# Kernel tuning notes

Hardware: AMD Instinct MI355X
Metric: run time of the kernel (lower is better)

## Reference

```python
import jax, jax.numpy as jnp
import numpy as np

B, N, D = 4, 1024, 1024
H = 16
HD = D // H
FF = int(D * 2.0)
EPS = 1e-5


def setup_inputs() -> dict:
    key = jax.random.key(0)
    ks = jax.random.split(key, 12)
    s = lambda fan_in: 1.0 / np.sqrt(fan_in)
    return {
        "x": jax.random.normal(ks[0], (B, N, D), dtype=jnp.float32),
        "ln1_g": jnp.ones((D,), jnp.float32),
        "ln1_b": jnp.zeros((D,), jnp.float32),
        "qkv_w": jax.random.normal(ks[1], (D, 3 * D), jnp.float32) * s(D),
        "qkv_b": jnp.zeros((3 * D,), jnp.float32),
        "out_w": jax.random.normal(ks[2], (D, D), jnp.float32) * s(D),
        "out_b": jnp.zeros((D,), jnp.float32),
        "ln2_g": jnp.ones((D,), jnp.float32),
        "ln2_b": jnp.zeros((D,), jnp.float32),
        "w1": jax.random.normal(ks[3], (D, FF), jnp.float32) * s(D),
        "b1": jnp.zeros((FF,), jnp.float32),
        "w2": jax.random.normal(ks[4], (FF, D), jnp.float32) * s(FF),
        "b2": jnp.zeros((D,), jnp.float32),
    }


def _layernorm(x, g, b):
    mu = jnp.mean(x, axis=-1, keepdims=True)
    var = jnp.mean(jnp.square(x - mu), axis=-1, keepdims=True)
    return (x - mu) * jax.lax.rsqrt(var + EPS) * g + b


def _attention(x, qkv_w, qkv_b, out_w, out_b):
    qkv = x @ qkv_w + qkv_b                       # (B,N,3D)
    qkv = qkv.reshape(B, N, 3, H, HD)
    q, k, v = qkv[:, :, 0], qkv[:, :, 1], qkv[:, :, 2]  # (B,N,H,HD)
    scale = 1.0 / np.sqrt(HD)
    attn = jnp.einsum("bnhd,bmhd->bhnm", q, k) * scale
    attn = jax.nn.softmax(attn, axis=-1)
    out = jnp.einsum("bhnm,bmhd->bnhd", attn, v).reshape(B, N, D)
    return out @ out_w + out_b


def reference(x, ln1_g, ln1_b, qkv_w, qkv_b, out_w, out_b, ln2_g, ln2_b, w1, b1, w2, b2):
    x = x + _attention(_layernorm(x, ln1_g, ln1_b), qkv_w, qkv_b, out_w, out_b)
    h = _layernorm(x, ln2_g, ln2_b)
    h = jax.nn.gelu(h @ w1 + b1, approximate=False) @ w2 + b2
    return x + h
```

## Files before the change

### kernel.cpp

```cpp
#include <hip/hip_runtime.h>
#include <hip/hip_bf16.h>
#include <cstdint>
#include <cstddef>

#define Bq 4
#define Nseq 1024
#define Dm 1024
#define Hh 16
#define HDd 64
#define FFd 2048
#define Mrows 4096

typedef __attribute__((ext_vector_type(8))) short bf16x8;
typedef __attribute__((ext_vector_type(4))) float f32x4;
typedef __attribute__((ext_vector_type(16))) float f32x16;

__device__ __forceinline__ void gl_lds16(const void* g, void* l) {
  __builtin_amdgcn_global_load_lds(
      (const __attribute__((address_space(1))) unsigned int*)g,
      (__attribute__((address_space(3))) unsigned int*)l, 16, 0, 0);
}

__device__ __forceinline__ unsigned short f2b(float f) {
  union { __hip_bfloat16 h; unsigned short u; } cv;
  cv.h = __float2bfloat16(f);
  return cv.u;
}

__device__ __forceinline__ unsigned cvt_pk_bf16(float a, float b) {
  unsigned r;
  asm("v_cvt_pk_bf16_f32 %0, %1, %2" : "=v"(r) : "v"(a), "v"(b));
  return r;
}

__device__ __forceinline__ void pl32_swap(unsigned& a, unsigned& b) {
  asm("v_permlane32_swap_b32 %0, %1" : "+v"(a), "+v"(b));
}

__global__ __launch_bounds__(256) void transpose_cast_k(
    const float* __restrict__ src, __hip_bfloat16* __restrict__ dst,
    int K, int Ncols) {
  __shared__ float tile[32][33];
  const int n0 = blockIdx.x * 32, k0 = blockIdx.y * 32;
  const int tx = threadIdx.x & 31, ty = threadIdx.x >> 5;
#pragma unroll
  for (int i = 0; i < 32; i += 8)
    tile[ty + i][tx] = src[(size_t)(k0 + ty + i) * Ncols + n0 + tx];
  __syncthreads();
#pragma unroll
  for (int i = 0; i < 32; i += 8)
    dst[(size_t)(n0 + ty + i) * K + k0 + tx] = __float2bfloat16(tile[tx][ty + i]);
}

__global__ __launch_bounds__(256) void ln_kernel(
    const float* __restrict__ x, const float* __restrict__ gw,
    const float* __restrict__ bw, __hip_bfloat16* __restrict__ out) {
  const int row = blockIdx.x;
  const float4 v = reinterpret_cast<const float4*>(x + (size_t)row * Dm)[threadIdx.x];
  float s1 = v.x + v.y + v.z + v.w;
  float s2 = v.x * v.x + v.y * v.y + v.z * v.z + v.w * v.w;
#pragma unroll
  for (int m = 1; m < 64; m <<= 1) {
    s1 += __shfl_xor(s1, m);
    s2 += __shfl_xor(s2, m);
  }
  __shared__ float a1[4], a2[4];
  const int wv = threadIdx.x >> 6;
  if ((threadIdx.x & 63) == 0) { a1[wv] = s1; a2[wv] = s2; }
  __syncthreads();
  s1 = a1[0] + a1[1] + a1[2] + a1[3];
  s2 = a2[0] + a2[1] + a2[2] + a2[3];
  const float mu = s1 * (1.f / Dm);
  const float rs = rsqrtf(s2 * (1.f / Dm) - mu * mu + 1e-5f);
  const float4 g4 = reinterpret_cast<const float4*>(gw)[threadIdx.x];
  const float4 b4 = reinterpret_cast<const float4*>(bw)[threadIdx.x];
  ushort4 o;
  o.x = f2b((v.x - mu) * rs * g4.x + b4.x);
  o.y = f2b((v.y - mu) * rs * g4.y + b4.y);
  o.z = f2b((v.z - mu) * rs * g4.z + b4.z);
  o.w = f2b((v.w - mu) * rs * g4.w + b4.w);
  reinterpret_cast<ushort4*>(out + (size_t)row * Dm)[threadIdx.x] = o;
}

template <int EPI>
__global__ __launch_bounds__(256, 3) void gemm_bt(
    const __hip_bfloat16* __restrict__ A, const __hip_bfloat16* __restrict__ BT,
    const float* __restrict__ bias, const float* __restrict__ res,
    float* __restrict__ outF, __hip_bfloat16* __restrict__ outB,
    __hip_bfloat16* __restrict__ qb, __hip_bfloat16* __restrict__ kb,
    __hip_bfloat16* __restrict__ vtb, int Ndim, int Kdim) {
  __shared__ alignas(16) __hip_bfloat16 As[128 * 64];
  __shared__ alignas(16) __hip_bfloat16 Bs[128 * 64];
  const int tid = threadIdx.x;
  const int wv = tid >> 6, ln = tid & 63;
  const int wm = wv >> 1, wn = wv & 1;
  const int lq = ln & 31, hl = ln >> 5;
  const int rowBase = blockIdx.y * 128;
  const int colBase = blockIdx.x * 128;

  const int st_row = tid >> 3;
  const int st_c = (tid & 7) ^ (st_row & 7);

  f32x16 acc[2][2];
#pragma unroll
  for (int i = 0; i < 2; ++i)
#pragma unroll
    for (int j = 0; j < 2; ++j) acc[i][j] = {};

  auto stage = [&](int k0) {
#pragma unroll
    for (int r = 0; r < 4; ++r) {
      gl_lds16(A + (size_t)(rowBase + r * 32 + st_row) * Kdim + k0 + st_c * 8,
               (char*)As + r * 4096 + wv * 1024);
      gl_lds16(BT + (size_t)(colBase + r * 32 + st_row) * Kdim + k0 + st_c * 8,
               (char*)Bs + r * 4096 + wv * 1024);
    }
  };

  const int nt = Kdim >> 6;
  for (int kt = 0; kt < nt; ++kt) {
    stage(kt << 6);
    __syncthreads();
    const char* Ap = (const char*)As;
    const char* Bp = (const char*)Bs;
#pragma unroll
    for (int ks = 0; ks < 4; ++ks) {
      bf16x8 af[2], bfr[2];
#pragma unroll
      for (int i = 0; i < 2; ++i)
        af[i] = *reinterpret_cast<const bf16x8*>(
            Ap + (wm * 64 + i * 32 + lq) * 128 + (((ks * 2 + hl) ^ (lq & 7)) * 16));
#pragma unroll
      for (int j = 0; j < 2; ++j)
        bfr[j] = *reinterpret_cast<const bf16x8*>(
            Bp + (wn * 64 + j * 32 + lq) * 128 + (((ks * 2 + hl) ^ (lq & 7)) * 16));
#pragma unroll
      for (int i = 0; i < 2; ++i)
#pragma unroll
        for (int j = 0; j < 2; ++j)
          acc[i][j] = __builtin_amdgcn_mfma_f32_32x32x16_bf16(af[i], bfr[j], acc[i][j], 0, 0, 0);
    }
    __syncthreads();
  }

#pragma unroll
  for (int i = 0; i < 2; ++i) {
#pragma unroll
    for (int j = 0; j < 2; ++j) {
      const int gc = colBase + wn * 64 + j * 32 + lq;
      const float bv = bias[gc];
#pragma unroll
      for (int r = 0; r < 16; ++r) {
        const int gr = rowBase + wm * 64 + i * 32 + (r & 3) + 8 * (r >> 2) + 4 * hl;
        float v = acc[i][j][r] + bv;
        if constexpr (EPI == 0) {
          const int which = gc >> 10;
          const int dcol = gc & 1023;
          const int h = dcol >> 6, hd = dcol & 63;
          const int b = gr >> 10, n = gr & 1023;
          const size_t bh = (size_t)(b * Hh + h);
          if (which == 0)
            qb[(bh * Nseq + n) * HDd + hd] = __float2bfloat16(v * 0.125f);
          else if (which == 1)
            kb[(bh * Nseq + n) * HDd + hd] = __float2bfloat16(v);
          else
            vtb[(bh * HDd + hd) * Nseq + n] = __float2bfloat16(v);
        } else if constexpr (EPI == 1) {
          outF[(size_t)gr * Ndim + gc] = v + res[(size_t)gr * Ndim + gc];
        } else {
          outB[(size_t)gr * Ndim + gc] =
              __float2bfloat16(0.5f * v * (1.f + erff(v * 0.70710678118f)));
        }
      }
    }
  }
}

__global__ __launch_bounds__(256, 2) void attn_kernel(
    const __hip_bfloat16* __restrict__ q, const __hip_bfloat16* __restrict__ k,
    const __hip_bfloat16* __restrict__ vt, __hip_bfloat16* __restrict__ attn) {
  __shared__ alignas(16) __hip_bfloat16 Ks[2][64 * 64];
  __shared__ alignas(16) __hip_bfloat16 Vs[2][64 * 64];
  const int tid = threadIdx.x, wv = tid >> 6, ln = tid & 63;
  const int bh = blockIdx.x >> 3, qt = blockIdx.x & 7;
  const int b = bh >> 4, h = bh & 15;
  const int lq = ln & 31;
  const int hl = ln >> 5;

  const __hip_bfloat16* kbase = k + (size_t)bh * Nseq * HDd;
  const __hip_bfloat16* vbase = vt + (size_t)bh * HDd * Nseq;

  const int st_r = ln >> 3;
  const int st_c = (ln & 7) ^ st_r;

  const __hip_bfloat16* qsrc = q + ((size_t)bh * Nseq + qt * 128 + wv * 32 + lq) * HDd;
  bf16x8 qf[4];
#pragma unroll
  for (int s = 0; s < 4; ++s)
    qf[s] = *reinterpret_cast<const bf16x8*>(qsrc + s * 16 + hl * 8);

  float mrun = -1e30f, lrun = 0.f;
  f32x16 ot0 = {}, ot1 = {};

  auto stage = [&](int buf, int kt) {
#pragma unroll
    for (int c = 0; c < 2; ++c) {
      const int chunk = wv * 2 + c;
      gl_lds16(kbase + ((size_t)kt * 64 + chunk * 8 + st_r) * HDd + st_c * 8,
               (char*)&Ks[buf][0] + chunk * 1024);
      gl_lds16(vbase + (size_t)(chunk * 8 + st_r) * Nseq + kt * 64 + st_c * 8,
               (char*)&Vs[buf][0] + chunk * 1024);
    }
  };

  stage(0, 0);
  __syncthreads();
  int cur = 0;

  for (int kt = 0; kt < 16; ++kt) {
    if (kt < 15) stage(cur ^ 1, kt + 1);

    const char* Kp = (const char*)&Ks[cur][0];
    const char* Vp = (const char*)&Vs[cur][0];

    f32x16 st0 = {}, st1 = {};
#pragma unroll
    for (int t = 0; t < 2; ++t) {
      const int row = t * 32 + lq;
#pragma unroll
      for (int s = 0; s < 4; ++s) {
        const bf16x8 kf = *reinterpret_cast<const bf16x8*>(
            Kp + row * 128 + (((s * 2 + hl) ^ (row & 7)) * 16));
        if (t == 0) st0 = __builtin_amdgcn_mfma_f32_32x32x16_bf16(kf, qf[s], st0, 0, 0, 0);
        else        st1 = __builtin_amdgcn_mfma_f32_32x32x16_bf16(kf, qf[s], st1, 0, 0, 0);
      }
    }

    float tmax = st0[0];
#pragma unroll
    for (int r = 1; r < 16; ++r) tmax = fmaxf(tmax, st0[r]);
#pragma unroll
    for (int r = 0; r < 16; ++r) tmax = fmaxf(tmax, st1[r]);
    tmax = fmaxf(tmax, __shfl_xor(tmax, 32));
    const float mn = fmaxf(mrun, tmax);
    const float sc = __expf(mrun - mn);
    mrun = mn;
    float tsum = 0.f;
#pragma unroll
    for (int r = 0; r < 16; ++r) {
      st0[r] = __expf(st0[r] - mn);
      tsum += st0[r];
    }
#pragma unroll
    for (int r = 0; r < 16; ++r) {
      st1[r] = __expf(st1[r] - mn);
      tsum += st1[r];
    }
    tsum += __shfl_xor(tsum, 32);
    lrun = lrun * sc + tsum;
#pragma unroll
    for (int r = 0; r < 16; ++r) { ot0[r] *= sc; ot1[r] *= sc; }

    union PF { unsigned u[4]; bf16x8 v; } pf[4];
#pragma unroll
    for (int t = 0; t < 2; ++t)
#pragma unroll
      for (int g = 0; g < 2; ++g) {
        unsigned w0, w1, w2, w3;
        if (t == 0) {
          w0 = cvt_pk_bf16(st0[g * 8 + 0], st0[g * 8 + 1]);
          w1 = cvt_pk_bf16(st0[g * 8 + 2], st0[g * 8 + 3]);
          w2 = cvt_pk_bf16(st0[g * 8 + 4], st0[g * 8 + 5]);
          w3 = cvt_pk_bf16(st0[g * 8 + 6], st0[g * 8 + 7]);
        } else {
          w0 = cvt_pk_bf16(st1[g * 8 + 0], st1[g * 8 + 1]);
          w1 = cvt_pk_bf16(st1[g * 8 + 2], st1[g * 8 + 3]);
          w2 = cvt_pk_bf16(st1[g * 8 + 4], st1[g * 8 + 5]);
          w3 = cvt_pk_bf16(st1[g * 8 + 6], st1[g * 8 + 7]);
        }
        pl32_swap(w0, w2);
        pl32_swap(w1, w3);
        PF f;
        f.u[0] = w0; f.u[1] = w1; f.u[2] = w2; f.u[3] = w3;
        pf[t * 2 + g] = f;
      }

#pragma unroll
    for (int dt = 0; dt < 2; ++dt) {
      const int row = dt * 32 + lq;
#pragma unroll
      for (int ks = 0; ks < 4; ++ks) {
        const bf16x8 vf = *reinterpret_cast<const bf16x8*>(
            Vp + row * 128 + (((ks * 2 + hl) ^ (row & 7)) * 16));
        if (dt == 0) ot0 = __builtin_amdgcn_mfma_f32_32x32x16_bf16(vf, pf[ks].v, ot0, 0, 0, 0);
        else         ot1 = __builtin_amdgcn_mfma_f32_32x32x16_bf16(vf, pf[ks].v, ot1, 0, 0, 0);
      }
    }

    __syncthreads();
    cur ^= 1;
  }

  const float inv = 1.f / lrun;
  char* swb = (char*)(&Ks[0][0] + wv * 2048);
#pragma unroll
  for (int dt = 0; dt < 2; ++dt)
#pragma unroll
    for (int i = 0; i < 8; ++i) {
      const unsigned w = (dt == 0)
          ? cvt_pk_bf16(ot0[2 * i] * inv, ot0[2 * i + 1] * inv)
          : cvt_pk_bf16(ot1[2 * i] * inv, ot1[2 * i + 1] * inv);
      const int d0 = (2 * i & 2) + 8 * (i >> 1) + 4 * hl + 32 * dt;
      *(unsigned*)(swb + lq * 128 + (((d0 >> 3) ^ (lq & 7)) * 16) + (d0 & 7) * 2) = w;
    }
  const int brow = b * Nseq + qt * 128 + wv * 32;
#pragma unroll
  for (int it = 0; it < 4; ++it) {
    const int qr = it * 8 + (ln >> 3);
    const bf16x8 o = *reinterpret_cast<const bf16x8*>(
        swb + qr * 128 + (((ln & 7) ^ (qr & 7)) * 16));
    *reinterpret_cast<bf16x8*>(attn + (size_t)(brow + qr) * Dm + h * 64 + (ln & 7) * 8) = o;
  }
}

extern "C" void kernel_launch(void* const* d_in, const int* in_sizes, int n_in,
                              void* d_out, int out_size, void* d_ws, size_t ws_size,
                              hipStream_t stream) {
  (void)in_sizes; (void)n_in; (void)out_size; (void)ws_size;
  const float* x     = (const float*)d_in[0];
  const float* ln1_g = (const float*)d_in[1];
  const float* ln1_b = (const float*)d_in[2];
  const float* qkv_w = (const float*)d_in[3];
  const float* qkv_b = (const float*)d_in[4];
  const float* out_w = (const float*)d_in[5];
  const float* out_b = (const float*)d_in[6];
  const float* ln2_g = (const float*)d_in[7];
  const float* ln2_b = (const float*)d_in[8];
  const float* w1    = (const float*)d_in[9];
  const float* b1    = (const float*)d_in[10];
  const float* w2    = (const float*)d_in[11];
  const float* b2    = (const float*)d_in[12];
  float* outp = (float*)d_out;

  char* ws = (char*)d_ws;
  size_t off = 0;
  auto take = [&](size_t bytes) {
    char* p = ws + off;
    off += (bytes + 255) & ~(size_t)255;
    return p;
  };
  __hip_bfloat16* wqkv_t = (__hip_bfloat16*)take((size_t)3 * Dm * Dm * 2);
  __hip_bfloat16* wout_t = (__hip_bfloat16*)take((size_t)Dm * Dm * 2);
  __hip_bfloat16* w1_t   = (__hip_bfloat16*)take((size_t)FFd * Dm * 2);
  __hip_bfloat16* w2_t   = (__hip_bfloat16*)take((size_t)Dm * FFd * 2);
  __hip_bfloat16* xn     = (__hip_bfloat16*)take((size_t)Mrows * Dm * 2);
  __hip_bfloat16* qb     = (__hip_bfloat16*)take((size_t)Mrows * Dm * 2);
  __hip_bfloat16* kb     = (__hip_bfloat16*)take((size_t)Mrows * Dm * 2);
  __hip_bfloat16* vtb    = (__hip_bfloat16*)take((size_t)Mrows * Dm * 2);
  __hip_bfloat16* attn   = (__hip_bfloat16*)take((size_t)Mrows * Dm * 2);
  float*          x1     = (float*)take((size_t)Mrows * Dm * 4);
  __hip_bfloat16* gbuf   = (__hip_bfloat16*)take((size_t)Mrows * FFd * 2);

  const dim3 blk(256);
  transpose_cast_k<<<dim3(3 * Dm / 32, Dm / 32), blk, 0, stream>>>(qkv_w, wqkv_t, Dm, 3 * Dm);
  transpose_cast_k<<<dim3(Dm / 32, Dm / 32), blk, 0, stream>>>(out_w, wout_t, Dm, Dm);
  transpose_cast_k<<<dim3(FFd / 32, Dm / 32), blk, 0, stream>>>(w1, w1_t, Dm, FFd);
  transpose_cast_k<<<dim3(Dm / 32, FFd / 32), blk, 0, stream>>>(w2, w2_t, FFd, Dm);
  ln_kernel<<<dim3(Mrows), blk, 0, stream>>>(x, ln1_g, ln1_b, xn);
  gemm_bt<0><<<dim3(3 * Dm / 128, Mrows / 128), blk, 0, stream>>>(
      xn, wqkv_t, qkv_b, nullptr, nullptr, nullptr, qb, kb, vtb, 3 * Dm, Dm);
  attn_kernel<<<dim3(Bq * Hh * (Nseq / 128)), blk, 0, stream>>>(qb, kb, vtb, attn);
  gemm_bt<1><<<dim3(Dm / 128, Mrows / 128), blk, 0, stream>>>(
      attn, wout_t, out_b, x, x1, nullptr, nullptr, nullptr, nullptr, Dm, Dm);
  ln_kernel<<<dim3(Mrows), blk, 0, stream>>>(x1, ln2_g, ln2_b, xn);
  gemm_bt<2><<<dim3(FFd / 128, Mrows / 128), blk, 0, stream>>>(
      xn, w1_t, b1, nullptr, nullptr, gbuf, nullptr, nullptr, nullptr, FFd, Dm);
  gemm_bt<1><<<dim3(Dm / 128, Mrows / 128), blk, 0, stream>>>(
      gbuf, w2_t, b2, x1, outp, nullptr, nullptr, nullptr, nullptr, Dm, FFd);
}
```

Before: 191.7 us.

## Double-buffer GEMM LDS tiles with K-step of 32 to overlap loads and MFMA

Converts the single-buffered 64-wide K tile into two 32-wide LDS buffers so the next tile's global-to-LDS loads are issued before computing on the current one. This removes one barrier per iteration and aims to hide global load latency behind MFMA work. The LDS layout and XOR swizzle are rewritten for 64-byte rows. The trade-off is twice as many loop iterations with half the MFMA work each, and reliance on the single barrier to order both buffer reuse and load completion.

```diff
diff --git a/kernel.cpp b/kernel.cpp
--- a/kernel.cpp
+++ b/kernel.cpp
@@ -89,8 +89,8 @@
     float* __restrict__ outF, __hip_bfloat16* __restrict__ outB,
     __hip_bfloat16* __restrict__ qb, __hip_bfloat16* __restrict__ kb,
     __hip_bfloat16* __restrict__ vtb, int Ndim, int Kdim) {
-  __shared__ alignas(16) __hip_bfloat16 As[128 * 64];
-  __shared__ alignas(16) __hip_bfloat16 Bs[128 * 64];
+  __shared__ alignas(16) __hip_bfloat16 As[2][128 * 32];
+  __shared__ alignas(16) __hip_bfloat16 Bs[2][128 * 32];
   const int tid = threadIdx.x;
   const int wv = tid >> 6, ln = tid & 63;
   const int wm = wv >> 1, wn = wv & 1;
@@ -98,8 +98,9 @@
   const int rowBase = blockIdx.y * 128;
   const int colBase = blockIdx.x * 128;
 
-  const int st_row = tid >> 3;
-  const int st_c = (tid & 7) ^ (st_row & 7);
+  const int st_row = wv * 16 + (ln >> 2);
+  const int st_lc  = (ln & 3) ^ ((ln >> 3) & 3);
+  const int rsw    = (lq >> 1) & 3;
 
   f32x16 acc[2][2];
 #pragma unroll
@@ -107,33 +108,36 @@
 #pragma unroll
     for (int j = 0; j < 2; ++j) acc[i][j] = {};
 
-  auto stage = [&](int k0) {
-#pragma unroll
-    for (int r = 0; r < 4; ++r) {
-      gl_lds16(A + (size_t)(rowBase + r * 32 + st_row) * Kdim + k0 + st_c * 8,
-               (char*)As + r * 4096 + wv * 1024);
-      gl_lds16(BT + (size_t)(colBase + r * 32 + st_row) * Kdim + k0 + st_c * 8,
-               (char*)Bs + r * 4096 + wv * 1024);
+  auto stage = [&](int buf, int k0) {
+#pragma unroll
+    for (int r = 0; r < 2; ++r) {
+      gl_lds16(A + (size_t)(rowBase + r * 64 + st_row) * Kdim + k0 + st_lc * 8,
+               (char*)&As[buf][0] + r * 4096 + wv * 1024);
+      gl_lds16(BT + (size_t)(colBase + r * 64 + st_row) * Kdim + k0 + st_lc * 8,
+               (char*)&Bs[buf][0] + r * 4096 + wv * 1024);
     }
   };
 
-  const int nt = Kdim >> 6;
+  const int nt = Kdim >> 5;
+  stage(0, 0);
+  __syncthreads();
+  int cur = 0;
+
   for (int kt = 0; kt < nt; ++kt) {
-    stage(kt << 6);
-    __syncthreads();
-    const char* Ap = (const char*)As;
-    const char* Bp = (const char*)Bs;
-#pragma unroll
-    for (int ks = 0; ks < 4; ++ks) {
+    if (kt + 1 < nt) stage(cur ^ 1, (kt + 1) << 5);
+    const char* Ap = (const char*)&As[cur][0];
+    const char* Bp = (const char*)&Bs[cur][0];
+#pragma unroll
+    for (int ks = 0; ks < 2; ++ks) {
       bf16x8 af[2], bfr[2];
 #pragma unroll
       for (int i = 0; i < 2; ++i)
         af[i] = *reinterpret_cast<const bf16x8*>(
-            Ap + (wm * 64 + i * 32 + lq) * 128 + (((ks * 2 + hl) ^ (lq & 7)) * 16));
+            Ap + (wm * 64 + i * 32 + lq) * 64 + (((ks * 2 + hl) ^ rsw) * 16));
 #pragma unroll
       for (int j = 0; j < 2; ++j)
         bfr[j] = *reinterpret_cast<const bf16x8*>(
-            Bp + (wn * 64 + j * 32 + lq) * 128 + (((ks * 2 + hl) ^ (lq & 7)) * 16));
+            Bp + (wn * 64 + j * 32 + lq) * 64 + (((ks * 2 + hl) ^ rsw) * 16));
 #pragma unroll
       for (int i = 0; i < 2; ++i)
 #pragma unroll
@@ -141,6 +145,7 @@
           acc[i][j] = __builtin_amdgcn_mfma_f32_32x32x16_bf16(af[i], bfr[j], acc[i][j], 0, 0, 0);
     }
     __syncthreads();
+    cur ^= 1;
   }
 
 #pragma unroll
```

New measurement: 204.3 us. +6.6%, slower.

## Merge weight prep and LN1 into one launch; use 64-row tiles for N=1024 GEMMs

Applied to the files above, without the earlier changes.

Fuses the four weight transpose-cast launches and the first layernorm into a single prep kernel indexed by block id, which removes launch overhead and tail gaps between the small kernels. Adds a gemm_sk kernel with 64x128 tiles for the two output-width-1024 GEMMs (out projection and FFN down), doubling the block count from 256 to 512 so the GPU's compute units are better filled. The trade-off is that the smaller tiles reuse less data and the new kernel is single-buffered with no prefetch.

```diff
diff --git a/kernel.cpp b/kernel.cpp
--- a/kernel.cpp
+++ b/kernel.cpp
@@ -37,12 +37,12 @@
   asm("v_permlane32_swap_b32 %0, %1" : "+v"(a), "+v"(b));
 }
 
-__global__ __launch_bounds__(256) void transpose_cast_k(
-    const float* __restrict__ src, __hip_bfloat16* __restrict__ dst,
-    int K, int Ncols) {
+__device__ __forceinline__ void tr_tile(const float* __restrict__ src,
+                                        __hip_bfloat16* __restrict__ dst,
+                                        int K, int Ncols, int n0, int k0,
+                                        int tid) {
   __shared__ float tile[32][33];
-  const int n0 = blockIdx.x * 32, k0 = blockIdx.y * 32;
-  const int tx = threadIdx.x & 31, ty = threadIdx.x >> 5;
+  const int tx = tid & 31, ty = tid >> 5;
 #pragma unroll
   for (int i = 0; i < 32; i += 8)
     tile[ty + i][tx] = src[(size_t)(k0 + ty + i) * Ncols + n0 + tx];
@@ -50,6 +50,54 @@
 #pragma unroll
   for (int i = 0; i < 32; i += 8)
     dst[(size_t)(n0 + ty + i) * K + k0 + tx] = __float2bfloat16(tile[tx][ty + i]);
+}
+
+__global__ __launch_bounds__(256) void prep_kernel(
+    const float* __restrict__ qkv_w, __hip_bfloat16* __restrict__ wqkv_t,
+    const float* __restrict__ out_w, __hip_bfloat16* __restrict__ wout_t,
+    const float* __restrict__ w1, __hip_bfloat16* __restrict__ w1_t,
+    const float* __restrict__ w2, __hip_bfloat16* __restrict__ w2_t,
+    const float* __restrict__ x, const float* __restrict__ ln1_g,
+    const float* __restrict__ ln1_b, __hip_bfloat16* __restrict__ xn) {
+  const int id = blockIdx.x, tid = threadIdx.x;
+  if (id < 3072) {
+    tr_tile(qkv_w, wqkv_t, Dm, 3 * Dm, (id % 96) * 32, (id / 96) * 32, tid);
+  } else if (id < 4096) {
+    const int i2 = id - 3072;
+    tr_tile(out_w, wout_t, Dm, Dm, (i2 % 32) * 32, (i2 / 32) * 32, tid);
+  } else if (id < 6144) {
+    const int i2 = id - 4096;
+    tr_tile(w1, w1_t, Dm, FFd, (i2 % 64) * 32, (i2 / 64) * 32, tid);
+  } else if (id < 8192) {
+    const int i2 = id - 6144;
+    tr_tile(w2, w2_t, FFd, Dm, (i2 % 32) * 32, (i2 / 32) * 32, tid);
+  } else {
+    const int row = id - 8192;
+    const float4 v = reinterpret_cast<const float4*>(x + (size_t)row * Dm)[tid];
+    float s1 = v.x + v.y + v.z + v.w;
+    float s2 = v.x * v.x + v.y * v.y + v.z * v.z + v.w * v.w;
+#pragma unroll
+    for (int m = 1; m < 64; m <<= 1) {
+      s1 += __shfl_xor(s1, m);
+      s2 += __shfl_xor(s2, m);
+    }
+    __shared__ float a1[4], a2[4];
+    const int wv = tid >> 6;
+    if ((tid & 63) == 0) { a1[wv] = s1; a2[wv] = s2; }
+    __syncthreads();
+    s1 = a1[0] + a1[1] + a1[2] + a1[3];
+    s2 = a2[0] + a2[1] + a2[2] + a2[3];
+    const float mu = s1 * (1.f / Dm);
+    const float rs = rsqrtf(s2 * (1.f / Dm) - mu * mu + 1e-5f);
+    const float4 g4 = reinterpret_cast<const float4*>(ln1_g)[tid];
+    const float4 b4 = reinterpret_cast<const float4*>(ln1_b)[tid];
+    ushort4 o;
+    o.x = f2b((v.x - mu) * rs * g4.x + b4.x);
+    o.y = f2b((v.y - mu) * rs * g4.y + b4.y);
+    o.z = f2b((v.z - mu) * rs * g4.z + b4.z);
+    o.w = f2b((v.w - mu) * rs * g4.w + b4.w);
+    reinterpret_cast<ushort4*>(xn + (size_t)row * Dm)[tid] = o;
+  }
 }
 
 __global__ __launch_bounds__(256) void ln_kernel(
@@ -85,8 +133,8 @@
 template <int EPI>
 __global__ __launch_bounds__(256, 3) void gemm_bt(
     const __hip_bfloat16* __restrict__ A, const __hip_bfloat16* __restrict__ BT,
-    const float* __restrict__ bias, const float* __restrict__ res,
-    float* __restrict__ outF, __hip_bfloat16* __restrict__ outB,
+    const float* __restrict__ bias,
+    __hip_bfloat16* __restrict__ outB,
     __hip_bfloat16* __restrict__ qb, __hip_bfloat16* __restrict__ kb,
     __hip_bfloat16* __restrict__ vtb, int Ndim, int Kdim) {
   __shared__ alignas(16) __hip_bfloat16 As[128 * 64];
@@ -165,13 +213,74 @@
             kb[(bh * Nseq + n) * HDd + hd] = __float2bfloat16(v);
           else
             vtb[(bh * HDd + hd) * Nseq + n] = __float2bfloat16(v);
-        } else if constexpr (EPI == 1) {
-          outF[(size_t)gr * Ndim + gc] = v + res[(size_t)gr * Ndim + gc];
         } else {
           outB[(size_t)gr * Ndim + gc] =
               __float2bfloat16(0.5f * v * (1.f + erff(v * 0.70710678118f)));
         }
       }
+    }
+  }
+}
+
+__global__ __launch_bounds__(256, 4) void gemm_sk(
+    const __hip_bfloat16* __restrict__ A, const __hip_bfloat16* __restrict__ BT,
+    const float* __restrict__ bias, const float* __restrict__ res,
+    float* __restrict__ outF, int Ndim, int Kdim) {
+  __shared__ alignas(16) __hip_bfloat16 As[64 * 64];
+  __shared__ alignas(16) __hip_bfloat16 Bs[128 * 64];
+  const int tid = threadIdx.x;
+  const int wv = tid >> 6, ln = tid & 63;
+  const int wm = wv >> 1, wn = wv & 1;
+  const int lq = ln & 31, hl = ln >> 5;
+  const int rowBase = blockIdx.y * 64;
+  const int colBase = blockIdx.x * 128;
+
+  const int st_row = tid >> 3;
+  const int st_c = (tid & 7) ^ (st_row & 7);
+
+  f32x16 acc[2];
+  acc[0] = {}; acc[1] = {};
+
+  auto stage = [&](int k0) {
+#pragma unroll
+    for (int r = 0; r < 2; ++r)
+      gl_lds16(A + (size_t)(rowBase + r * 32 + st_row) * Kdim + k0 + st_c * 8,
+               (char*)As + r * 4096 + wv * 1024);
+#pragma unroll
+    for (int r = 0; r < 4; ++r)
+      gl_lds16(BT + (size_t)(colBase + r * 32 + st_row) * Kdim + k0 + st_c * 8,
+               (char*)Bs + r * 4096 + wv * 1024);
+  };
+
+  const int nt = Kdim >> 6;
+  for (int kt = 0; kt < nt; ++kt) {
+    stage(kt << 6);
+    __syncthreads();
+    const char* Ap = (const char*)As;
+    const char* Bp = (const char*)Bs;
+#pragma unroll
+    for (int ks = 0; ks < 4; ++ks) {
+      const int csw = ((ks * 2 + hl) ^ (lq & 7)) * 16;
+      const bf16x8 af = *reinterpret_cast<const bf16x8*>(
+          Ap + (wm * 32 + lq) * 128 + csw);
+#pragma unroll
+      for (int j = 0; j < 2; ++j) {
+        const bf16x8 bfr = *reinterpret_cast<const bf16x8*>(
+            Bp + (wn * 64 + j * 32 + lq) * 128 + csw);
+        acc[j] = __builtin_amdgcn_mfma_f32_32x32x16_bf16(af, bfr, acc[j], 0, 0, 0);
+      }
+    }
+    __syncthreads();
+  }
+
+#pragma unroll
+  for (int j = 0; j < 2; ++j) {
+    const int gc = colBase + wn * 64 + j * 32 + lq;
+    const float bv = bias[gc];
+#pragma unroll
+    for (int r = 0; r < 16; ++r) {
+      const int gr = rowBase + wm * 32 + (r & 3) + 8 * (r >> 2) + 4 * hl;
+      outF[(size_t)gr * Ndim + gc] = acc[j][r] + bv + res[(size_t)gr * Ndim + gc];
     }
   }
 }
@@ -362,19 +471,16 @@
   __hip_bfloat16* gbuf   = (__hip_bfloat16*)take((size_t)Mrows * FFd * 2);
 
   const dim3 blk(256);
-  transpose_cast_k<<<dim3(3 * Dm / 32, Dm / 32), blk, 0, stream>>>(qkv_w, wqkv_t, Dm, 3 * Dm);
-  transpose_cast_k<<<dim3(Dm / 32, Dm / 32), blk, 0, stream>>>(out_w, wout_t, Dm, Dm);
-  transpose_cast_k<<<dim3(FFd / 32, Dm / 32), blk, 0, stream>>>(w1, w1_t, Dm, FFd);
-  transpose_cast_k<<<dim3(Dm / 32, FFd / 32), blk, 0, stream>>>(w2, w2_t, FFd, Dm);
-  ln_kernel<<<dim3(Mrows), blk, 0, stream>>>(x, ln1_g, ln1_b, xn);
+  prep_kernel<<<dim3(12288), blk, 0, stream>>>(
+      qkv_w, wqkv_t, out_w, wout_t, w1, w1_t, w2, w2_t, x, ln1_g, ln1_b, xn);
   gemm_bt<0><<<dim3(3 * Dm / 128, Mrows / 128), blk, 0, stream>>>(
-      xn, wqkv_t, qkv_b, nullptr, nullptr, nullptr, qb, kb, vtb, 3 * Dm, Dm);
+      xn, wqkv_t, qkv_b, nullptr, qb, kb, vtb, 3 * Dm, Dm);
   attn_kernel<<<dim3(Bq * Hh * (Nseq / 128)), blk, 0, stream>>>(qb, kb, vtb, attn);
-  gemm_bt<1><<<dim3(Dm / 128, Mrows / 128), blk, 0, stream>>>(
-      attn, wout_t, out_b, x, x1, nullptr, nullptr, nullptr, nullptr, Dm, Dm);
+  gemm_sk<<<dim3(Dm / 128, Mrows / 64), blk, 0, stream>>>(
+      attn, wout_t, out_b, x, x1, Dm, Dm);
   ln_kernel<<<dim3(Mrows), blk, 0, stream>>>(x1, ln2_g, ln2_b, xn);
   gemm_bt<2><<<dim3(FFd / 128, Mrows / 128), blk, 0, stream>>>(
-      xn, w1_t, b1, nullptr, nullptr, gbuf, nullptr, nullptr, nullptr, FFd, Dm);
-  gemm_bt<1><<<dim3(Dm / 128, Mrows / 128), blk, 0, stream>>>(
-      gbuf, w2_t, b2, x1, outp, nullptr, nullptr, nullptr, nullptr, Dm, FFd);
-}
+      xn, w1_t, b1, gbuf, nullptr, nullptr, nullptr, FFd, Dm);
+  gemm_sk<<<dim3(Dm / 128, Mrows / 64), blk, 0, stream>>>(
+      gbuf, w2_t, b2, x1, outp, Dm, FFd);
+}
```

Result: faster. 177.1 us (-7.6%).
